# Kernel optimization log

Hardware: AMD Instinct MI355X
Metric: run time of the kernel (lower is better)

## Reference

```python
import jax, jax.numpy as jnp
import numpy as np


def setup_inputs() -> dict:
    key = jax.random.key(0)
    k1, k2 = jax.random.split(key)
    N, D = 16384, 512
    image_features = jax.random.normal(k1, (N, D), dtype=jnp.float32)
    text_features = jax.random.normal(k2, (N, D), dtype=jnp.float32)
    # CLIP typically learns log-scale init exp(log(1/0.07)) ~ 14.28; use 1.0*exp-like scale
    logit_scale = jnp.asarray(14.285714, dtype=jnp.float32)
    return {"image_features": image_features, "text_features": text_features, "logit_scale": logit_scale}


def reference(image_features, text_features, logit_scale):
    # logits_per_image: [N, N]; logits_per_text is its transpose (world_size=1)
    logits_per_image = logit_scale * jnp.einsum("nd,md->nm", image_features, text_features)
    logits_per_text = logits_per_image.T
    n = logits_per_image.shape[0]
    labels = jnp.arange(n)
    # cross_entropy with labels == diagonal: mean over rows of (logsumexp(row) - row[label])
    lse_i = jax.nn.logsumexp(logits_per_image, axis=-1)
    lse_t = jax.nn.logsumexp(logits_per_text, axis=-1)
    diag = jnp.diagonal(logits_per_image)  # logits_per_image[i,i] == logits_per_text[i,i]
    loss_i = jnp.mean(lse_i - diag)
    loss_t = jnp.mean(lse_t - diag)
    return (loss_i + loss_t) / 2
```

## Files before the change

kernel.cpp:

```cpp
#include <hip/hip_runtime.h>
#include <hip/hip_bf16.h>
#include <stdint.h>

#define NR 16384
#define DIM 512
#define BK 32
#define NT (DIM / BK)
#define NTILE (NR / 256)
#define TILE_US (256 * BK)

typedef __bf16 bf16x8 __attribute__((ext_vector_type(8)));
typedef float f32x4 __attribute__((ext_vector_type(4)));

__device__ inline ushort f2bf(float x) {
  uint32_t u = __float_as_uint(x);
  uint32_t r = (u + 0x7FFFu + ((u >> 16) & 1u)) >> 16;
  return (ushort)r;
}

__global__ __launch_bounds__(256) void convert_diag(
    const float* __restrict__ I, const float* __restrict__ T,
    const float* __restrict__ scale_p,
    ushort* __restrict__ bI, ushort* __restrict__ bT,
    float* __restrict__ diag)
{
  int wid = threadIdx.x >> 6;
  int lane = threadIdx.x & 63;
  int row = blockIdx.x * 4 + wid;
  const float4* I4 = (const float4*)(I + (size_t)row * DIM);
  const float4* T4 = (const float4*)(T + (size_t)row * DIM);
  ushort* bIr = bI + (size_t)row * DIM;
  ushort* bTr = bT + (size_t)row * DIM;
  float dot = 0.f;
#pragma unroll
  for (int h = 0; h < 2; ++h) {
    int idx = lane + h * 64;
    float4 a = I4[idx];
    float4 b = T4[idx];
    dot += a.x * b.x + a.y * b.y + a.z * b.z + a.w * b.w;
    ushort4 ha, hb;
    ha.x = f2bf(a.x); ha.y = f2bf(a.y); ha.z = f2bf(a.z); ha.w = f2bf(a.w);
    hb.x = f2bf(b.x); hb.y = f2bf(b.y); hb.z = f2bf(b.z); hb.w = f2bf(b.w);
    *(ushort4*)(bIr + (size_t)idx * 4) = ha;
    *(ushort4*)(bTr + (size_t)idx * 4) = hb;
  }
#pragma unroll
  for (int off = 32; off > 0; off >>= 1) dot += __shfl_down(dot, off);
  if (lane == 0) diag[row] = scale_p[0] * dot;
}

__global__ __launch_bounds__(512, 2) void gemm_lse(
    const ushort* __restrict__ bI, const ushort* __restrict__ bT,
    const float* __restrict__ scale_p,
    float2* __restrict__ rowPart, float2* __restrict__ colPart)
{
  __shared__ __align__(16) ushort As[3][TILE_US];
  __shared__ __align__(16) ushort Bs[3][TILE_US];

  int bid = blockIdx.x;
  int x = bid & 7, s = bid >> 3;
  int bi = x * 8 + (s & 7);
  int bj = s >> 3;

  int tid = threadIdx.x;
  int w = tid >> 6, lane = tid & 63;
  int wr = w >> 2, wc = w & 3;

  const ushort* gA = bI + (size_t)bi * 256 * DIM;
  const ushort* gB = bT + (size_t)bj * 256 * DIM;

  int srow = tid >> 2;
  int sslot = (tid & 3) ^ ((tid >> 3) & 3);

  auto stage = [&](ushort* dstTile, const ushort* srcMat, int kt, int h) {
    const ushort* g = srcMat + (size_t)(h * 128 + srow) * DIM + kt * BK + sslot * 8;
    ushort* d = dstTile + (h * 128 + w * 16) * BK;
    __builtin_amdgcn_global_load_lds(
        (const __attribute__((address_space(1))) void*)g,
        (__attribute__((address_space(3))) void*)d, 16, 0, 0);
  };

  f32x4 acc[8][4];
#pragma unroll
  for (int m = 0; m < 8; ++m)
#pragma unroll
    for (int n = 0; n < 4; ++n)
      acc[m][n] = (f32x4){0.f, 0.f, 0.f, 0.f};

  stage(As[0], gA, 0, 0); stage(As[0], gA, 0, 1);
  stage(Bs[0], gB, 0, 0); stage(Bs[0], gB, 0, 1);
  stage(As[1], gA, 1, 0); stage(As[1], gA, 1, 1);
  stage(Bs[1], gB, 1, 0); stage(Bs[1], gB, 1, 1);
  asm volatile("s_waitcnt vmcnt(4)" ::: "memory");
  __builtin_amdgcn_sched_barrier(0);
  __builtin_amdgcn_s_barrier();

  int aRow0 = wr * 128 + (lane & 15);
  int bRow0 = wc * 64 + (lane & 15);
  int sLog = lane >> 4;

  auto ldFrag = [&](const ushort* tile, int row) -> bf16x8 {
    int off = row * (BK * 2) + ((sLog ^ ((row >> 1) & 3)) << 4);
    return *(const bf16x8*)((const char*)tile + off);
  };

  int buf = 0, nb = 2;
  for (int t = 0; t < NT; ++t) {
    const ushort* At = As[buf];
    const ushort* Bt = Bs[buf];
    ushort* An = As[nb];
    ushort* Bn = Bs[nb];
    bool pf = (t + 2 < NT);

    bf16x8 aF[4], bF[4], aG[4];
#pragma unroll
    for (int m = 0; m < 4; ++m) aF[m] = ldFrag(At, aRow0 + m * 16);
#pragma unroll
    for (int n = 0; n < 4; ++n) bF[n] = ldFrag(Bt, bRow0 + n * 16);
    if (pf) { stage(An, gA, t + 2, 0); stage(An, gA, t + 2, 1); }
    __builtin_amdgcn_sched_barrier(0);
    __builtin_amdgcn_s_setprio(1);
#pragma unroll
    for (int m = 0; m < 4; ++m)
#pragma unroll
      for (int n = 0; n < 4; ++n)
        acc[m][n] = __builtin_amdgcn_mfma_f32_16x16x32_bf16(aF[m], bF[n], acc[m][n], 0, 0, 0);
    __builtin_amdgcn_s_setprio(0);
    __builtin_amdgcn_sched_barrier(0);

#pragma unroll
    for (int m = 0; m < 4; ++m) aG[m] = ldFrag(At, aRow0 + 64 + m * 16);
    if (pf) { stage(Bn, gB, t + 2, 0); stage(Bn, gB, t + 2, 1); }
    __builtin_amdgcn_sched_barrier(0);
    __builtin_amdgcn_s_setprio(1);
#pragma unroll
    for (int m = 0; m < 4; ++m)
#pragma unroll
      for (int n = 0; n < 4; ++n)
        acc[m + 4][n] = __builtin_amdgcn_mfma_f32_16x16x32_bf16(aG[m], bF[n], acc[m + 4][n], 0, 0, 0);
    __builtin_amdgcn_s_setprio(0);

    if (pf) asm volatile("s_waitcnt vmcnt(4)" ::: "memory");
    else    asm volatile("s_waitcnt vmcnt(0)" ::: "memory");
    __builtin_amdgcn_sched_barrier(0);
    __builtin_amdgcn_s_barrier();

    buf = (buf == 2) ? 0 : buf + 1;
    nb  = (nb == 2) ? 0 : nb + 1;
  }

  float sc = scale_p[0];
#pragma unroll
  for (int m = 0; m < 8; ++m)
#pragma unroll
    for (int n = 0; n < 4; ++n)
      acc[m][n] *= sc;

  float2* redRow = (float2*)&As[0][0];
  float2* redCol = (float2*)&Bs[0][0];

#pragma unroll
  for (int m = 0; m < 8; ++m) {
#pragma unroll
    for (int j = 0; j < 4; ++j) {
      float rm = fmaxf(fmaxf(acc[m][0][j], acc[m][1][j]),
                       fmaxf(acc[m][2][j], acc[m][3][j]));
#pragma unroll
      for (int msk = 1; msk <= 8; msk <<= 1) rm = fmaxf(rm, __shfl_xor(rm, msk));
      float rs = 0.f;
#pragma unroll
      for (int n = 0; n < 4; ++n) rs += __expf(acc[m][n][j] - rm);
#pragma unroll
      for (int msk = 1; msk <= 8; msk <<= 1) rs += __shfl_xor(rs, msk);
      if ((lane & 15) == 0) {
        int r = wr * 128 + m * 16 + (lane >> 4) * 4 + j;
        redRow[r * 4 + wc] = make_float2(rm, rs);
      }
    }
  }
#pragma unroll
  for (int n = 0; n < 4; ++n) {
    float cm = -1e30f;
#pragma unroll
    for (int m = 0; m < 8; ++m)
#pragma unroll
      for (int j = 0; j < 4; ++j) cm = fmaxf(cm, acc[m][n][j]);
    cm = fmaxf(cm, __shfl_xor(cm, 16));
    cm = fmaxf(cm, __shfl_xor(cm, 32));
    float cs = 0.f;
#pragma unroll
    for (int m = 0; m < 8; ++m)
#pragma unroll
      for (int j = 0; j < 4; ++j) cs += __expf(acc[m][n][j] - cm);
    cs += __shfl_xor(cs, 16);
    cs += __shfl_xor(cs, 32);
    if (lane < 16) {
      int c = wc * 64 + n * 16 + lane;
      redCol[c * 2 + wr] = make_float2(cm, cs);
    }
  }
  __syncthreads();

  if (tid < 256) {
    float2 p = redRow[tid * 4];
    float m_ = p.x, s_ = p.y;
#pragma unroll
    for (int q = 1; q < 4; ++q) {
      float2 r = redRow[tid * 4 + q];
      float mn = fmaxf(m_, r.x);
      s_ = s_ * __expf(m_ - mn) + r.y * __expf(r.x - mn);
      m_ = mn;
    }
    rowPart[(size_t)bj * NR + bi * 256 + tid] = make_float2(m_, s_);
  } else {
    int c = tid - 256;
    float2 p0 = redCol[c * 2], p1 = redCol[c * 2 + 1];
    float mn = fmaxf(p0.x, p1.x);
    float s_ = p0.y * __expf(p0.x - mn) + p1.y * __expf(p1.x - mn);
    colPart[(size_t)bi * NR + bj * 256 + c] = make_float2(mn, s_);
  }
}

__global__ __launch_bounds__(256) void reduce_final(
    const float2* __restrict__ rowPart, const float2* __restrict__ colPart,
    const float* __restrict__ diag, float* __restrict__ out)
{
  int bid = blockIdx.x;
  bool isCol = bid >= 64;
  int i = (bid & 63) * 256 + threadIdx.x;
  const float2* part = isCol ? colPart : rowPart;
  float m = -1e30f, s = 0.f;
  for (int b = 0; b < NTILE; ++b) {
    float2 p = part[(size_t)b * NR + i];
    float mn = fmaxf(m, p.x);
    s = s * __expf(m - mn) + p.y * __expf(p.x - mn);
    m = mn;
  }
  float contrib = (m + __logf(s)) - diag[i];
#pragma unroll
  for (int off = 32; off > 0; off >>= 1) contrib += __shfl_down(contrib, off);
  __shared__ float wsum[4];
  int wid = threadIdx.x >> 6, lane = threadIdx.x & 63;
  if (lane == 0) wsum[wid] = contrib;
  __syncthreads();
  if (threadIdx.x == 0) {
    float tot = wsum[0] + wsum[1] + wsum[2] + wsum[3];
    atomicAdd(out, tot * (1.0f / (2.0f * NR)));
  }
}

extern "C" void kernel_launch(void* const* d_in, const int* in_sizes, int n_in,
                              void* d_out, int out_size, void* d_ws, size_t ws_size,
                              hipStream_t stream) {
  const float* I = (const float*)d_in[0];
  const float* T = (const float*)d_in[1];
  const float* scale = (const float*)d_in[2];
  float* out = (float*)d_out;

  char* ws = (char*)d_ws;
  ushort* bI      = (ushort*)(ws);
  ushort* bT      = (ushort*)(ws + ((size_t)16 << 20));
  float2* rowPart = (float2*)(ws + ((size_t)32 << 20));
  float2* colPart = (float2*)(ws + ((size_t)48 << 20));
  float*  diag    = (float*) (ws + ((size_t)64 << 20));

  hipMemsetAsync(d_out, 0, sizeof(float), stream);
  convert_diag<<<NR / 4, 256, 0, stream>>>(I, T, scale, bI, bT, diag);
  gemm_lse<<<NTILE * NTILE, 512, 0, stream>>>(bI, bT, scale, rowPart, colPart);
  reduce_final<<<128, 256, 0, stream>>>(rowPart, colPart, diag, out);
}
```

Measured before the change: 514.5 us.

## Restructure GEMM mainloop into four-phase ping-pong schedule with BK=64 tiles

The K-tile grows from 32 to 64 and the triple-buffered LDS becomes a double buffer with an 8-slot XOR swizzle. Each iteration is split into four MFMA quadrants, with fragment loads, barriers and prefetch of the next-but-one tile interleaved between them. The aim is to halve the loop iteration count, overlap global-to-LDS staging with MFMA work and reduce LDS bank conflicts. In exchange it adds many more workgroup barriers per iteration and raises register pressure from holding 24 fragments.

```diff
diff --git a/kernel.cpp b/kernel.cpp
--- a/kernel.cpp
+++ b/kernel.cpp
@@ -4,10 +4,9 @@
 
 #define NR 16384
 #define DIM 512
-#define BK 32
-#define NT (DIM / BK)
+#define BK 64
+#define NT8 (DIM / BK)
 #define NTILE (NR / 256)
-#define TILE_US (256 * BK)
 
 typedef __bf16 bf16x8 __attribute__((ext_vector_type(8)));
 typedef float f32x4 __attribute__((ext_vector_type(4)));
@@ -17,6 +16,10 @@
   uint32_t r = (u + 0x7FFFu + ((u >> 16) & 1u)) >> 16;
   return (ushort)r;
 }
+
+#define MFMA __builtin_amdgcn_mfma_f32_16x16x32_bf16
+#define SB() __builtin_amdgcn_sched_barrier(0)
+#define BAR() __builtin_amdgcn_s_barrier()
 
 __global__ __launch_bounds__(256) void convert_diag(
     const float* __restrict__ I, const float* __restrict__ T,
@@ -54,8 +57,8 @@
     const float* __restrict__ scale_p,
     float2* __restrict__ rowPart, float2* __restrict__ colPart)
 {
-  __shared__ __align__(16) ushort As[3][TILE_US];
-  __shared__ __align__(16) ushort Bs[3][TILE_US];
+  __shared__ __align__(16) ushort As[2][2][128][64];
+  __shared__ __align__(16) ushort Bs[2][2][128][64];
 
   int bid = blockIdx.x;
   int x = bid & 7, s = bid >> 3;
@@ -69,15 +72,19 @@
   const ushort* gA = bI + (size_t)bi * 256 * DIM;
   const ushort* gB = bT + (size_t)bj * 256 * DIM;
 
-  int srow = tid >> 2;
-  int sslot = (tid & 3) ^ ((tid >> 3) & 3);
-
-  auto stage = [&](ushort* dstTile, const ushort* srcMat, int kt, int h) {
-    const ushort* g = srcMat + (size_t)(h * 128 + srow) * DIM + kt * BK + sslot * 8;
-    ushort* d = dstTile + (h * 128 + w * 16) * BK;
-    __builtin_amdgcn_global_load_lds(
-        (const __attribute__((address_space(1))) void*)g,
-        (__attribute__((address_space(3))) void*)d, 16, 0, 0);
+  int sslot3 = (tid & 7) ^ ((tid >> 3) & 7);
+  int srow = tid >> 3;
+
+  auto stageHalf = [&](ushort* dstHalf, const ushort* srcMat, int kt, int half) {
+#pragma unroll
+    for (int L = 0; L < 2; ++L) {
+      int row = L * 64 + srow;
+      const ushort* g = srcMat + (size_t)(half * 128 + row) * DIM + kt * BK + sslot3 * 8;
+      ushort* d = dstHalf + L * 4096 + w * 512;
+      __builtin_amdgcn_global_load_lds(
+          (const __attribute__((address_space(1))) void*)g,
+          (__attribute__((address_space(3))) void*)d, 16, 0, 0);
+    }
   };
 
   f32x4 acc[8][4];
@@ -87,66 +94,111 @@
     for (int n = 0; n < 4; ++n)
       acc[m][n] = (f32x4){0.f, 0.f, 0.f, 0.f};
 
-  stage(As[0], gA, 0, 0); stage(As[0], gA, 0, 1);
-  stage(Bs[0], gB, 0, 0); stage(Bs[0], gB, 0, 1);
-  stage(As[1], gA, 1, 0); stage(As[1], gA, 1, 1);
-  stage(Bs[1], gB, 1, 0); stage(Bs[1], gB, 1, 1);
-  asm volatile("s_waitcnt vmcnt(4)" ::: "memory");
-  __builtin_amdgcn_sched_barrier(0);
-  __builtin_amdgcn_s_barrier();
-
-  int aRow0 = wr * 128 + (lane & 15);
-  int bRow0 = wc * 64 + (lane & 15);
-  int sLog = lane >> 4;
-
-  auto ldFrag = [&](const ushort* tile, int row) -> bf16x8 {
-    int off = row * (BK * 2) + ((sLog ^ ((row >> 1) & 3)) << 4);
-    return *(const bf16x8*)((const char*)tile + off);
+  stageHalf(&As[0][0][0][0], gA, 0, 0); stageHalf(&As[0][1][0][0], gA, 0, 1);
+  stageHalf(&Bs[0][0][0][0], gB, 0, 0); stageHalf(&Bs[0][1][0][0], gB, 0, 1);
+  stageHalf(&Bs[1][0][0][0], gB, 1, 0); stageHalf(&Bs[1][1][0][0], gB, 1, 1);
+  stageHalf(&As[1][0][0][0], gA, 1, 0); stageHalf(&As[1][1][0][0], gA, 1, 1);
+  asm volatile("s_waitcnt vmcnt(8)" ::: "memory");
+  SB(); BAR(); SB();
+
+  int l15 = lane & 15, l7 = lane & 7, lq = lane >> 4;
+  auto fragOff = [&](int b16, int k) -> int {
+    int ks = k * 4 + lq;
+    return b16 * 2048 + l15 * 128 + ((ks ^ l7) << 4);
   };
 
-  int buf = 0, nb = 2;
-  for (int t = 0; t < NT; ++t) {
-    const ushort* At = As[buf];
-    const ushort* Bt = Bs[buf];
-    ushort* An = As[nb];
-    ushort* Bn = Bs[nb];
-    bool pf = (t + 2 < NT);
-
-    bf16x8 aF[4], bF[4], aG[4];
-#pragma unroll
-    for (int m = 0; m < 4; ++m) aF[m] = ldFrag(At, aRow0 + m * 16);
-#pragma unroll
-    for (int n = 0; n < 4; ++n) bF[n] = ldFrag(Bt, bRow0 + n * 16);
-    if (pf) { stage(An, gA, t + 2, 0); stage(An, gA, t + 2, 1); }
-    __builtin_amdgcn_sched_barrier(0);
+  for (int t = 0; t < NT8; ++t) {
+    int buf = t & 1;
+    const char* At = (const char*)&As[buf][wr][0][0];
+    const char* Bt = (const char*)&Bs[buf][wc >> 1][0][0] + (wc & 1) * 8192;
+    bool pf = (t + 2 < NT8);
+
+    bf16x8 aLo[8], aHi[8], bLo[4], bHi[4];
+
+#pragma unroll
+    for (int m = 0; m < 4; ++m)
+#pragma unroll
+      for (int k = 0; k < 2; ++k)
+        aLo[m * 2 + k] = *(const bf16x8*)(At + fragOff(m, k));
+#pragma unroll
+    for (int n = 0; n < 2; ++n)
+#pragma unroll
+      for (int k = 0; k < 2; ++k)
+        bLo[n * 2 + k] = *(const bf16x8*)(Bt + fragOff(n, k));
+    SB(); BAR();
+    asm volatile("s_waitcnt lgkmcnt(0)" ::: "memory");
+    SB();
     __builtin_amdgcn_s_setprio(1);
 #pragma unroll
     for (int m = 0; m < 4; ++m)
 #pragma unroll
-      for (int n = 0; n < 4; ++n)
-        acc[m][n] = __builtin_amdgcn_mfma_f32_16x16x32_bf16(aF[m], bF[n], acc[m][n], 0, 0, 0);
+      for (int n = 0; n < 2; ++n)
+#pragma unroll
+        for (int k = 0; k < 2; ++k)
+          acc[m][n] = MFMA(aLo[m * 2 + k], bLo[n * 2 + k], acc[m][n], 0, 0, 0);
     __builtin_amdgcn_s_setprio(0);
-    __builtin_amdgcn_sched_barrier(0);
-
-#pragma unroll
-    for (int m = 0; m < 4; ++m) aG[m] = ldFrag(At, aRow0 + 64 + m * 16);
-    if (pf) { stage(Bn, gB, t + 2, 0); stage(Bn, gB, t + 2, 1); }
-    __builtin_amdgcn_sched_barrier(0);
+    SB(); BAR(); SB();
+
+#pragma unroll
+    for (int n = 2; n < 4; ++n)
+#pragma unroll
+      for (int k = 0; k < 2; ++k)
+        bHi[(n - 2) * 2 + k] = *(const bf16x8*)(Bt + fragOff(n, k));
+    SB(); BAR();
+    asm volatile("s_waitcnt lgkmcnt(0)" ::: "memory");
+    SB();
     __builtin_amdgcn_s_setprio(1);
 #pragma unroll
     for (int m = 0; m < 4; ++m)
 #pragma unroll
-      for (int n = 0; n < 4; ++n)
-        acc[m + 4][n] = __builtin_amdgcn_mfma_f32_16x16x32_bf16(aG[m], bF[n], acc[m + 4][n], 0, 0, 0);
+      for (int n = 2; n < 4; ++n)
+#pragma unroll
+        for (int k = 0; k < 2; ++k)
+          acc[m][n] = MFMA(aLo[m * 2 + k], bHi[(n - 2) * 2 + k], acc[m][n], 0, 0, 0);
     __builtin_amdgcn_s_setprio(0);
-
-    if (pf) asm volatile("s_waitcnt vmcnt(4)" ::: "memory");
+    SB(); BAR(); SB();
+
+#pragma unroll
+    for (int m = 4; m < 8; ++m)
+#pragma unroll
+      for (int k = 0; k < 2; ++k)
+        aHi[(m - 4) * 2 + k] = *(const bf16x8*)(At + fragOff(m, k));
+    if (pf) {
+      stageHalf(&Bs[buf][0][0][0], gB, t + 2, 0);
+      stageHalf(&Bs[buf][1][0][0], gB, t + 2, 1);
+    }
+    SB(); BAR();
+    asm volatile("s_waitcnt lgkmcnt(0)" ::: "memory");
+    SB();
+    __builtin_amdgcn_s_setprio(1);
+#pragma unroll
+    for (int m = 4; m < 8; ++m)
+#pragma unroll
+      for (int n = 0; n < 2; ++n)
+#pragma unroll
+        for (int k = 0; k < 2; ++k)
+          acc[m][n] = MFMA(aHi[(m - 4) * 2 + k], bLo[n * 2 + k], acc[m][n], 0, 0, 0);
+    __builtin_amdgcn_s_setprio(0);
+    SB(); BAR(); SB();
+
+    if (pf) {
+      stageHalf(&As[buf][0][0][0], gA, t + 2, 0);
+      stageHalf(&As[buf][1][0][0], gA, t + 2, 1);
+    }
+    SB();
+    if (pf) asm volatile("s_waitcnt vmcnt(8)" ::: "memory");
     else    asm volatile("s_waitcnt vmcnt(0)" ::: "memory");
-    __builtin_amdgcn_sched_barrier(0);
-    __builtin_amdgcn_s_barrier();
-
-    buf = (buf == 2) ? 0 : buf + 1;
-    nb  = (nb == 2) ? 0 : nb + 1;
+    SB(); BAR(); SB();
+    __builtin_amdgcn_s_setprio(1);
+#pragma unroll
+    for (int m = 4; m < 8; ++m)
+#pragma unroll
+      for (int n = 2; n < 4; ++n)
+#pragma unroll
+        for (int k = 0; k < 2; ++k)
+          acc[m][n] = MFMA(aHi[(m - 4) * 2 + k], bHi[(n - 2) * 2 + k], acc[m][n], 0, 0, 0);
+    __builtin_amdgcn_s_setprio(0);
+    SB(); BAR(); SB();
   }
 
   float sc = scale_p[0];
@@ -156,8 +208,8 @@
     for (int n = 0; n < 4; ++n)
       acc[m][n] *= sc;
 
-  float2* redRow = (float2*)&As[0][0];
-  float2* redCol = (float2*)&Bs[0][0];
+  float2* redRow = (float2*)&As[0][0][0][0];
+  float2* redCol = (float2*)&Bs[0][0][0][0];
 
 #pragma unroll
   for (int m = 0; m < 8; ++m) {
```

Result: slower. 540.3 us (+5.0%).
